# Kernel tuning notes

Measured on AMD Instinct MI355X. Metric: run time of the kernel, lower is better.

## Reference

```python
import jax, jax.numpy as jnp
import numpy as np

DIM = 512
HEADS = 8
HEAD_DIM = 64
INNER = HEADS * HEAD_DIM  # 512
FF = DIM * 2
EPS = 1e-5


def layernorm(x, g, b):
    mu = jnp.mean(x, axis=-1, keepdims=True)
    var = jnp.var(x, axis=-1, keepdims=True)
    return (x - mu) * jax.lax.rsqrt(var + EPS) * g + b


def setup_inputs() -> dict:
    key = jax.random.key(0)
    ks = jax.random.split(key, 10)
    s = lambda fan_in: 1.0 / np.sqrt(fan_in)
    return {
        "x": jax.random.normal(ks[0], (4, 2048, DIM), dtype=jnp.float32),
        "ln1_g": jnp.ones((DIM,), jnp.float32),
        "ln1_b": jnp.zeros((DIM,), jnp.float32),
        "w_qkv": jax.random.normal(ks[1], (DIM, 3 * INNER), jnp.float32) * s(DIM),
        "w_out": jax.random.normal(ks[2], (INNER, DIM), jnp.float32) * s(INNER),
        "b_out": jnp.zeros((DIM,), jnp.float32),
        "ln2_g": jnp.ones((DIM,), jnp.float32),
        "ln2_b": jnp.zeros((DIM,), jnp.float32),
        "w1": jax.random.normal(ks[3], (DIM, FF), jnp.float32) * s(DIM),
        "b1": jnp.zeros((FF,), jnp.float32),
        "w2": jax.random.normal(ks[4], (FF, DIM), jnp.float32) * s(FF),
        "b2": jnp.zeros((DIM,), jnp.float32),
    }


def reference(x, ln1_g, ln1_b, w_qkv, w_out, b_out, ln2_g, ln2_b, w1, b1, w2, b2):
    b, n, _ = x.shape
    # --- pre-LN MHSA ---
    h = layernorm(x, ln1_g, ln1_b)
    qkv = h @ w_qkv  # [b, n, 3*inner]
    q, k, v = jnp.split(qkv, 3, axis=-1)
    to_heads = lambda t: t.reshape(b, n, HEADS, HEAD_DIM).transpose(0, 2, 1, 3)
    q, k, v = to_heads(q), to_heads(k), to_heads(v)
    scores = jnp.einsum('bhid,bhjd->bhij', q, k) * (HEAD_DIM ** -0.5)
    attn = jax.nn.softmax(scores, axis=-1)
    attended = jnp.einsum('bhij,bhjd->bhid', attn, v)
    attended = attended.transpose(0, 2, 1, 3).reshape(b, n, INNER)
    x = attended @ w_out + b_out + x
    # --- pre-LN MLP ---
    h = layernorm(x, ln2_g, ln2_b)
    h = jax.nn.gelu(h @ w1 + b1, approximate=False)
    x = h @ w2 + b2 + x
    return x
```

## Files before the change

### kernel.cpp

```cpp
#include <hip/hip_runtime.h>
#include <math.h>


#define TOKENS 8192
#define SEQ    2048
typedef unsigned short u16;
typedef __attribute__((ext_vector_type(8))) _Float16 h8;
typedef __attribute__((ext_vector_type(4))) float f32x4;
typedef __attribute__((ext_vector_type(4))) unsigned short u16x4;

__device__ __forceinline__ u16 f2h(float f) {
    _Float16 h = (_Float16)f;
    return __builtin_bit_cast(u16, h);
}
__device__ __forceinline__ unsigned int pk2h(float a, float b) {
    return __builtin_bit_cast(unsigned int, __builtin_amdgcn_cvt_pkrtz(a, b));
}
__device__ __forceinline__ void a16(void* lds, const void* g) {
    __builtin_amdgcn_global_load_lds(
        (const __attribute__((address_space(1))) unsigned int*)g,
        (__attribute__((address_space(3))) unsigned int*)lds, 16, 0, 0);
}
__device__ __forceinline__ float gelu_exact(float v) {
    return 0.5f * v * (1.0f + erff(v * 0.70710678118654752f));
}

__global__ __launch_bounds__(256) void prep_k(const float* __restrict__ wqkv,
                                              const float* __restrict__ wout,
                                              const float* __restrict__ w1,
                                              const float* __restrict__ w2,
                                              u16* __restrict__ dqkv,
                                              u16* __restrict__ dout,
                                              u16* __restrict__ d1,
                                              u16* __restrict__ d2,
                                              const float* __restrict__ x,
                                              const float* __restrict__ g,
                                              const float* __restrict__ bta,
                                              u16* __restrict__ oh) {
    const int tid = threadIdx.x;
    if (blockIdx.x >= 512) {
        const int lane = tid & 63;
        const int row  = ((blockIdx.x - 512) << 2) + (tid >> 6);
        const float* xr = x + ((size_t)row << 9) + (lane << 3);
        float v[8];
        *(float4*)&v[0] = *(const float4*)xr;
        *(float4*)&v[4] = *(const float4*)(xr + 4);
        float s = 0.f, ss = 0.f;
#pragma unroll
        for (int i = 0; i < 8; i++) { s += v[i]; ss += v[i] * v[i]; }
#pragma unroll
        for (int m = 32; m; m >>= 1) {
            s  += __shfl_xor(s, m, 64);
            ss += __shfl_xor(ss, m, 64);
        }
        const float mu   = s * (1.0f / 512.0f);
        const float rstd = rsqrtf(ss * (1.0f / 512.0f) - mu * mu + 1e-5f);
        float gg[8], bb[8];
        *(float4*)&gg[0] = *(const float4*)(g + (lane << 3));
        *(float4*)&gg[4] = *(const float4*)(g + (lane << 3) + 4);
        *(float4*)&bb[0] = *(const float4*)(bta + (lane << 3));
        *(float4*)&bb[4] = *(const float4*)(bta + (lane << 3) + 4);
        union { u16 us[8]; uint4 q; } H;
#pragma unroll
        for (int i = 0; i < 8; i++) H.us[i] = f2h((v[i] - mu) * rstd * gg[i] + bb[i]);
        *(uint4*)&oh[((size_t)row << 9) + (lane << 3)] = H.q;
        return;
    }
    __shared__ float t[64][65];
    int b = blockIdx.x;
    const float* src; u16* dst; int K, N, n0, k0;
    if (b < 192)      { src = wqkv; dst = dqkv; K = 512;  N = 1536; n0 = (b % 24) << 6; k0 = (b / 24) << 6; }
    else if (b < 256) { b -= 192; src = wout; dst = dout; K = 512;  N = 512;  n0 = (b & 7) << 6;  k0 = (b >> 3) << 6; }
    else if (b < 384) { b -= 256; src = w1;   dst = d1;   K = 512;  N = 1024; n0 = (b & 15) << 6; k0 = (b >> 4) << 6; }
    else              { b -= 384; src = w2;   dst = d2;   K = 1024; N = 512;  n0 = (b & 7) << 6;  k0 = (b >> 3) << 6; }
    {
        const int kr = tid >> 2, nc = (tid & 3) << 4;
        const float* p = src + (size_t)(k0 + kr) * N + n0 + nc;
#pragma unroll
        for (int i = 0; i < 4; i++)
            *(float4*)&t[kr][nc + (i << 2)] = *(const float4*)(p + (i << 2));
    }
    __syncthreads();
    {
        const int nr = tid >> 2, kc = (tid & 3) << 4;
        union { u16 us[16]; uint4 q[2]; } H;
#pragma unroll
        for (int i = 0; i < 16; i++) H.us[i] = f2h(t[kc + i][nr]);
        const size_t o = (size_t)(n0 + nr) * K + k0 + kc;
        *(uint4*)&dst[o] = H.q[0];
        *(uint4*)&dst[o + 8] = H.q[1];
    }
}

__global__ __launch_bounds__(256) void ln_k(const float* __restrict__ x,
                                            const float* __restrict__ g,
                                            const float* __restrict__ bta,
                                            u16* __restrict__ oh) {
    const int lane = threadIdx.x & 63;
    const int row  = (blockIdx.x << 2) + (threadIdx.x >> 6);
    const float* xr = x + ((size_t)row << 9) + (lane << 3);
    float v[8];
    *(float4*)&v[0] = *(const float4*)xr;
    *(float4*)&v[4] = *(const float4*)(xr + 4);
    float s = 0.f, ss = 0.f;
#pragma unroll
    for (int i = 0; i < 8; i++) { s += v[i]; ss += v[i] * v[i]; }
#pragma unroll
    for (int m = 32; m; m >>= 1) {
        s  += __shfl_xor(s, m, 64);
        ss += __shfl_xor(ss, m, 64);
    }
    const float mu   = s * (1.0f / 512.0f);
    const float rstd = rsqrtf(ss * (1.0f / 512.0f) - mu * mu + 1e-5f);
    float gg[8], bb[8];
    *(float4*)&gg[0] = *(const float4*)(g + (lane << 3));
    *(float4*)&gg[4] = *(const float4*)(g + (lane << 3) + 4);
    *(float4*)&bb[0] = *(const float4*)(bta + (lane << 3));
    *(float4*)&bb[4] = *(const float4*)(bta + (lane << 3) + 4);
    union { u16 us[8]; uint4 q; } H;
#pragma unroll
    for (int i = 0; i < 8; i++) H.us[i] = f2h((v[i] - mu) * rstd * gg[i] + bb[i]);
    *(uint4*)&oh[((size_t)row << 9) + (lane << 3)] = H.q;
}

template <int EPI>
__global__ __launch_bounds__(256, 3) void sgemm_k(
    const u16* __restrict__ A, const u16* __restrict__ B,
    const float* __restrict__ bias, const float* __restrict__ res,
    float* __restrict__ Cf, u16* __restrict__ Ch, u16* __restrict__ Dh,
    int M, int N, int K) {
    __shared__ u16 sm[24576];
    const int tid = threadIdx.x;
    const int lane = tid & 63, wv = tid >> 6;
    const int col = lane & 15, quad = lane >> 4;
    const int wm = (wv & 1) << 6, wn = (wv >> 1) << 6;
    const int bm = blockIdx.y << 7, bn = blockIdx.x << 7;

    const int r0 = tid >> 2,         c0 = (tid & 3) ^ ((r0 >> 1) & 3);
    const int r1 = (tid + 256) >> 2, c1 = (tid & 3) ^ ((r1 >> 1) & 3);
    const u16* Ag0 = A + (size_t)(bm + r0) * K + c0 * 8;
    const u16* Ag1 = A + (size_t)(bm + r1) * K + c1 * 8;
    const u16* Bg0 = B + (size_t)(bn + r0) * K + c0 * 8;
    const u16* Bg1 = B + (size_t)(bn + r1) * K + c1 * 8;
    const int lw0 = wv * 512, lw1 = wv * 512 + 2048;
    const int swz = (col >> 1) & 3;
    const f32x4 z4 = {0.f, 0.f, 0.f, 0.f};
    f32x4 acc[4][4] = {{z4,z4,z4,z4},{z4,z4,z4,z4},{z4,z4,z4,z4},{z4,z4,z4,z4}};

    a16(&sm[lw0],        Ag0);       a16(&sm[lw1],        Ag1);
    a16(&sm[lw0 + 4096], Bg0);       a16(&sm[lw1 + 4096], Bg1);
    a16(&sm[8192 + lw0],        Ag0 + 32);  a16(&sm[8192 + lw1],        Ag1 + 32);
    a16(&sm[8192 + lw0 + 4096], Bg0 + 32);  a16(&sm[8192 + lw1 + 4096], Bg1 + 32);

    int cb = 0;
    int nb = 16384;
    for (int k0 = 0; k0 < K; k0 += 32) {
        if (k0 + 32 < K) {
            asm volatile("s_waitcnt vmcnt(4) lgkmcnt(0)\n\ts_barrier" ::: "memory");
        } else {
            asm volatile("s_waitcnt vmcnt(0) lgkmcnt(0)\n\ts_barrier" ::: "memory");
        }
        if (k0 + 64 < K) {
            const int kn = k0 + 64;
            a16(&sm[nb + lw0],        Ag0 + kn);  a16(&sm[nb + lw1],        Ag1 + kn);
            a16(&sm[nb + lw0 + 4096], Bg0 + kn);  a16(&sm[nb + lw1 + 4096], Bg1 + kn);
        }
        h8 af[4];
#pragma unroll
        for (int mt = 0; mt < 4; mt++) {
            const int ra = cb + (wm + (mt << 4) + col) * 32 + ((quad ^ swz) << 3);
            af[mt] = *(const h8*)&sm[ra];
        }
#pragma unroll
        for (int nt = 0; nt < 4; nt++) {
            const int rb = cb + 4096 + (wn + (nt << 4) + col) * 32 + ((quad ^ swz) << 3);
            h8 bf = *(const h8*)&sm[rb];
#pragma unroll
            for (int mt = 0; mt < 4; mt++)
                acc[mt][nt] = __builtin_amdgcn_mfma_f32_16x16x32_f16(af[mt], bf, acc[mt][nt], 0, 0, 0);
        }
        nb = cb;
        cb = (cb == 16384) ? 0 : cb + 8192;
    }

    if constexpr (EPI == 0) {
        if (bn >= 1024) {
            const int hd0  = (bn - 1024) >> 6;
            const int b8   = (bm >> 11) << 3;
            const int keyb = bm & 2047;
            __syncthreads();
#pragma unroll
            for (int hf = 0; hf < 2; hf++) {
                if ((wv >> 1) == hf) {
#pragma unroll
                    for (int mt = 0; mt < 4; mt++)
#pragma unroll
                    for (int rr = 0; rr < 4; rr++) {
                        const int key = wm + (mt << 4) + (quad << 2) + rr;
#pragma unroll
                        for (int nt = 0; nt < 4; nt++) {
                            const int dl = (nt << 4) + col;
                            sm[dl * 136 + key] = f2h(acc[mt][nt][rr]);
                        }
                    }
                }
                __syncthreads();
                {
                    const int d = tid >> 2;
#pragma unroll
                    for (int c = 0; c < 4; c++) {
                        const int key0 = ((((tid & 3) << 2) + c) << 3);
                        const size_t gb = ((size_t)(b8 + hd0 + hf) << 17)
                                        + ((size_t)d << 11) + keyb + key0;
                        *(uint4*)&Dh[gb] = *(const uint4*)&sm[d * 136 + key0];
                    }
                }
                __syncthreads();
            }
            return;
        }
    }

    float bs[4];
    if constexpr (EPI >= 1) {
#pragma unroll
        for (int nt = 0; nt < 4; nt++) bs[nt] = bias[bn + wn + (nt << 4) + col];
    }
#pragma unroll
    for (int mt = 0; mt < 4; mt++) {
#pragma unroll
        for (int rr = 0; rr < 4; rr++) {
            const int row = bm + wm + (mt << 4) + (quad << 2) + rr;
#pragma unroll
            for (int nt = 0; nt < 4; nt++) {
                const int colg = bn + wn + (nt << 4) + col;
                float v = acc[mt][nt][rr];
                if constexpr (EPI == 0) {
                    const int b = row >> 11, key = row & 2047;
                    if (bn < 512) {
                        Cf[((size_t)row << 9) + colg] = v;
                    } else {
                        const int hd = (colg - 512) >> 6, d = colg & 63;
                        Ch[((size_t)((b << 3) + hd) << 17) + (key << 6) + d] = f2h(v);
                    }
                } else if constexpr (EPI == 2) {
                    Ch[(size_t)row * N + colg] = f2h(gelu_exact(v + bs[nt]));
                } else {
                    const size_t o = (size_t)row * N + colg;
                    Cf[o] = v + bs[nt] + res[o];
                }
            }
        }
    }
}

__global__ __launch_bounds__(256, 4) void attn_k(const float* __restrict__ q,
                                                 const u16* __restrict__ kh,
                                                 const u16* __restrict__ vth,
                                                 u16* __restrict__ ah) {
    __shared__ u16 sm[20480];
    const int tid = threadIdx.x;
    const int lane = tid & 63, wv = tid >> 6;
    const int col = lane & 15, quad = lane >> 4;
    const int qt = blockIdx.x, bh = blockIdx.y;
    const int b = bh >> 3, h = bh & 7;
    const size_t tok0 = (size_t)b * SEQ;
    const size_t bhK = (size_t)bh << 17;
    const int q0 = qt << 6;

    h8 qf[2];
    {
        const int qrow = q0 + (wv << 4) + col;
        const float* qp = q + ((tok0 + qrow) << 9) + (h << 6) + (quad << 3);
#pragma unroll
        for (int kc = 0; kc < 2; kc++) {
            float v[8];
            *(float4*)&v[0] = *(const float4*)(qp + (kc << 5));
            *(float4*)&v[4] = *(const float4*)(qp + (kc << 5) + 4);
            union { u16 us[8]; h8 v8; } H;
#pragma unroll
            for (int i = 0; i < 8; i++) H.us[i] = f2h(v[i] * 0.125f);
            qf[kc] = H.v8;
        }
    }

    const f32x4 z4 = {0.f, 0.f, 0.f, 0.f};
    f32x4 o[4] = {z4, z4, z4, z4};
    float m_run = -1e30f, l_run = 0.f;

    size_t kbz[2], vbz[2];
    int doff[2];
#pragma unroll
    for (int j = 0; j < 2; j++) {
        const int C = (((j << 2) + wv) << 6) + lane;
        const int sr = C >> 3, sp = (C & 7) ^ (sr & 7);
        kbz[j] = bhK + ((size_t)sr << 6) + (sp << 3);
        vbz[j] = bhK + ((size_t)sr << 11) + (sp << 3);
        doff[j] = (((j << 2) + wv) << 9);
    }

#pragma unroll
    for (int j = 0; j < 2; j++) a16(&sm[doff[j]], kh + kbz[j]);
#pragma unroll
    for (int j = 0; j < 2; j++) a16(&sm[8192 + doff[j]], vth + vbz[j]);
#pragma unroll
    for (int j = 0; j < 2; j++) a16(&sm[4096 + doff[j]], kh + kbz[j] + 4096);

    int ib = 0;
    const int prow = (wv << 4) + col;
    const int p64 = prow << 6, p7 = prow & 7;
    for (int jt = 0; jt < 32; jt++, ib ^= 1) {
        if (jt < 31) {
            asm volatile("s_waitcnt vmcnt(2) lgkmcnt(0)\n\ts_barrier" ::: "memory");
        } else {
            asm volatile("s_waitcnt vmcnt(0) lgkmcnt(0)\n\ts_barrier" ::: "memory");
        }
        if (jt < 31) {
            const size_t vo = (size_t)(jt + 1) << 6;
            const int vb = 8192 + ((ib ^ 1) << 12);
#pragma unroll
            for (int j = 0; j < 2; j++) a16(&sm[vb + doff[j]], vth + vbz[j] + vo);
        }

        const int cb = ib << 12;
        f32x4 st[4] = {z4, z4, z4, z4};
        __builtin_amdgcn_s_setprio(1);
#pragma unroll
        for (int kb = 0; kb < 4; kb++) {
            const int key = (kb << 4) + col;
            const int r64 = key << 6, k7 = key & 7;
#pragma unroll
            for (int kc = 0; kc < 2; kc++) {
                const int ofs = cb + r64 + ((((kc << 2) + quad) ^ k7) << 3);
                h8 kf = *(const h8*)&sm[ofs];
                st[kb] = __builtin_amdgcn_mfma_f32_16x16x32_f16(kf, qf[kc], st[kb], 0, 0, 0);
            }
        }
        __builtin_amdgcn_s_setprio(0);

        float mx = st[0][0];
#pragma unroll
        for (int kb = 0; kb < 4; kb++)
#pragma unroll
            for (int r = 0; r < 4; r++) mx = fmaxf(mx, st[kb][r]);
        mx = fmaxf(mx, __shfl_xor(mx, 16));
        mx = fmaxf(mx, __shfl_xor(mx, 32));
        if (__any(mx > m_run + 7.5f)) {
            const float mn  = fmaxf(m_run, mx);
            const float alp = __expf(m_run - mn);
            m_run = mn;
            l_run *= alp;
            float aO[4];
#pragma unroll
            for (int r = 0; r < 4; r++) aO[r] = __shfl(alp, (quad << 2) + r);
#pragma unroll
            for (int db = 0; db < 4; db++) {
                o[db][0] *= aO[0]; o[db][1] *= aO[1];
                o[db][2] *= aO[2]; o[db][3] *= aO[3];
            }
        }
        float p[16];
        float rs = 0.0f;
#pragma unroll
        for (int kb = 0; kb < 4; kb++)
#pragma unroll
            for (int r = 0; r < 4; r++) {
                float e = __expf(st[kb][r] - m_run);
                p[(kb << 2) + r] = e;
                rs += e;
            }
        rs += __shfl_xor(rs, 16);
        rs += __shfl_xor(rs, 32);
        l_run += rs;
#pragma unroll
        for (int kb = 0; kb < 4; kb++) {
            uint2 w;
            w.x = pk2h(p[(kb << 2) + 0], p[(kb << 2) + 1]);
            w.y = pk2h(p[(kb << 2) + 2], p[(kb << 2) + 3]);
            const int c = (kb << 1) + (quad >> 1);
            *(uint2*)&sm[16384 + p64 + ((c ^ p7) << 3) + ((quad & 1) << 2)] = w;
        }

        asm volatile("s_waitcnt lgkmcnt(0)\n\ts_barrier" ::: "memory");

        if (jt < 30) {
            const size_t ko = (size_t)(jt + 2) << 12;
            const int kb2 = ib << 12;
#pragma unroll
            for (int j = 0; j < 2; j++) a16(&sm[kb2 + doff[j]], kh + kbz[j] + ko);
        }

        h8 pf[2];
#pragma unroll
        for (int kc = 0; kc < 2; kc++)
            pf[kc] = *(const h8*)&sm[16384 + p64 + ((((kc << 2) + quad) ^ p7) << 3)];

        const int vbase = 8192 + (ib << 12);
        __builtin_amdgcn_s_setprio(1);
#pragma unroll
        for (int db = 0; db < 4; db++) {
            const int d = (db << 4) + col;
            const int v64 = vbase + (d << 6), d7 = d & 7;
#pragma unroll
            for (int kc = 0; kc < 2; kc++) {
                h8 vf = *(const h8*)&sm[v64 + ((((kc << 2) + quad) ^ d7) << 3)];
                o[db] = __builtin_amdgcn_mfma_f32_16x16x32_f16(pf[kc], vf, o[db], 0, 0, 0);
            }
        }
        __builtin_amdgcn_s_setprio(0);
    }

    float linv[4];
#pragma unroll
    for (int r = 0; r < 4; r++) linv[r] = 1.0f / __shfl(l_run, (quad << 2) + r);
#pragma unroll
    for (int r = 0; r < 4; r++) {
        const size_t rowo = ((tok0 + q0 + (wv << 4) + (quad << 2) + r) << 9)
                            + (h << 6) + col;
#pragma unroll
        for (int db = 0; db < 4; db++)
            ah[rowo + (db << 4)] = f2h(o[db][r] * linv[r]);
    }
}

extern "C" void kernel_launch(void* const* d_in, const int* in_sizes, int n_in,
                              void* d_out, int out_size, void* d_ws, size_t ws_size,
                              hipStream_t stream) {
    const float* x     = (const float*)d_in[0];
    const float* ln1_g = (const float*)d_in[1];
    const float* ln1_b = (const float*)d_in[2];
    const float* w_qkv = (const float*)d_in[3];
    const float* w_out = (const float*)d_in[4];
    const float* b_out = (const float*)d_in[5];
    const float* ln2_g = (const float*)d_in[6];
    const float* ln2_b = (const float*)d_in[7];
    const float* w1    = (const float*)d_in[8];
    const float* b1    = (const float*)d_in[9];
    const float* w2    = (const float*)d_in[10];
    const float* b2    = (const float*)d_in[11];
    float* out = (float*)d_out;

    u16* wqkvh = (u16*)d_ws;
    u16* wouth = wqkvh + 1536 * 512;
    u16* w1h   = wouth + 512 * 512;
    u16* w2h   = w1h + 1024 * 512;
    u16* hbuf  = w2h + 512 * 1024;
    float* qbuf = (float*)(hbuf + (size_t)TOKENS * 512);
    float* x2   = qbuf;
    u16* kh  = (u16*)(qbuf + (size_t)TOKENS * 512);
    u16* vth = kh + (size_t)32 * 131072;
    u16* gh  = kh;

    prep_k<<<2560, 256, 0, stream>>>(w_qkv, w_out, w1, w2, wqkvh, wouth, w1h, w2h,
                                     x, ln1_g, ln1_b, hbuf);
    sgemm_k<0><<<dim3(12, 64), 256, 0, stream>>>(hbuf, wqkvh, nullptr, nullptr,
                                                 qbuf, kh, vth, TOKENS, 1536, 512);
    attn_k<<<dim3(32, 32), 256, 0, stream>>>(qbuf, kh, vth, hbuf);
    sgemm_k<1><<<dim3(4, 64), 256, 0, stream>>>(hbuf, wouth, b_out, x,
                                                x2, nullptr, nullptr, TOKENS, 512, 512);
    ln_k<<<TOKENS / 4, 256, 0, stream>>>(x2, ln2_g, ln2_b, hbuf);
    sgemm_k<2><<<dim3(8, 64), 256, 0, stream>>>(hbuf, w1h, b1, nullptr,
                                                nullptr, gh, nullptr, TOKENS, 1024, 512);
    sgemm_k<3><<<dim3(4, 64), 256, 0, stream>>>(gh, w2h, b2, x2,
                                                out, nullptr, nullptr, TOKENS, 512, 1024);
}
```

Baseline: 238.2 us.

## Double attention query tile per block to reuse K/V loads across two subtiles

Each attention block now handles 128 query rows instead of 64, with every wave processing two 16-row subtiles that share each K and V fragment read from shared memory. This halves the K/V global-to-LDS traffic and the barrier count per query row. In exchange the grid halves to 512 blocks, register pressure rises (launch bounds reduced to 2 blocks per SM), and the LDS buffer grows to hold the larger P tile.

```diff
diff --git a/kernel.cpp b/kernel.cpp
--- a/kernel.cpp
+++ b/kernel.cpp
@@ -254,11 +254,11 @@
     }
 }
 
-__global__ __launch_bounds__(256, 4) void attn_k(const float* __restrict__ q,
+__global__ __launch_bounds__(256, 2) void attn_k(const float* __restrict__ q,
                                                  const u16* __restrict__ kh,
                                                  const u16* __restrict__ vth,
                                                  u16* __restrict__ ah) {
-    __shared__ u16 sm[20480];
+    __shared__ u16 sm[24576];
     const int tid = threadIdx.x;
     const int lane = tid & 63, wv = tid >> 6;
     const int col = lane & 15, quad = lane >> 4;
@@ -266,11 +266,12 @@
     const int b = bh >> 3, h = bh & 7;
     const size_t tok0 = (size_t)b * SEQ;
     const size_t bhK = (size_t)bh << 17;
-    const int q0 = qt << 6;
-
-    h8 qf[2];
-    {
-        const int qrow = q0 + (wv << 4) + col;
+    const int q0 = qt << 7;
+
+    h8 qf[2][2];
+#pragma unroll
+    for (int sub = 0; sub < 2; sub++) {
+        const int qrow = q0 + (wv << 5) + (sub << 4) + col;
         const float* qp = q + ((tok0 + qrow) << 9) + (h << 6) + (quad << 3);
 #pragma unroll
         for (int kc = 0; kc < 2; kc++) {
@@ -280,13 +281,13 @@
             union { u16 us[8]; h8 v8; } H;
 #pragma unroll
             for (int i = 0; i < 8; i++) H.us[i] = f2h(v[i] * 0.125f);
-            qf[kc] = H.v8;
+            qf[sub][kc] = H.v8;
         }
     }
 
     const f32x4 z4 = {0.f, 0.f, 0.f, 0.f};
-    f32x4 o[4] = {z4, z4, z4, z4};
-    float m_run = -1e30f, l_run = 0.f;
+    f32x4 o[2][4] = {{z4, z4, z4, z4}, {z4, z4, z4, z4}};
+    float m_run[2] = {-1e30f, -1e30f}, l_run[2] = {0.f, 0.f};
 
     size_t kbz[2], vbz[2];
     int doff[2];
@@ -307,8 +308,6 @@
     for (int j = 0; j < 2; j++) a16(&sm[4096 + doff[j]], kh + kbz[j] + 4096);
 
     int ib = 0;
-    const int prow = (wv << 4) + col;
-    const int p64 = prow << 6, p7 = prow & 7;
     for (int jt = 0; jt < 32; jt++, ib ^= 1) {
         if (jt < 31) {
             asm volatile("s_waitcnt vmcnt(2) lgkmcnt(0)\n\ts_barrier" ::: "memory");
@@ -323,7 +322,7 @@
         }
 
         const int cb = ib << 12;
-        f32x4 st[4] = {z4, z4, z4, z4};
+        f32x4 st0[4] = {z4, z4, z4, z4}, st1[4] = {z4, z4, z4, z4};
         __builtin_amdgcn_s_setprio(1);
 #pragma unroll
         for (int kb = 0; kb < 4; kb++) {
@@ -333,52 +332,59 @@
             for (int kc = 0; kc < 2; kc++) {
                 const int ofs = cb + r64 + ((((kc << 2) + quad) ^ k7) << 3);
                 h8 kf = *(const h8*)&sm[ofs];
-                st[kb] = __builtin_amdgcn_mfma_f32_16x16x32_f16(kf, qf[kc], st[kb], 0, 0, 0);
+                st0[kb] = __builtin_amdgcn_mfma_f32_16x16x32_f16(kf, qf[0][kc], st0[kb], 0, 0, 0);
+                st1[kb] = __builtin_amdgcn_mfma_f32_16x16x32_f16(kf, qf[1][kc], st1[kb], 0, 0, 0);
             }
         }
         __builtin_amdgcn_s_setprio(0);
 
-        float mx = st[0][0];
-#pragma unroll
-        for (int kb = 0; kb < 4; kb++)
-#pragma unroll
-            for (int r = 0; r < 4; r++) mx = fmaxf(mx, st[kb][r]);
-        mx = fmaxf(mx, __shfl_xor(mx, 16));
-        mx = fmaxf(mx, __shfl_xor(mx, 32));
-        if (__any(mx > m_run + 7.5f)) {
-            const float mn  = fmaxf(m_run, mx);
-            const float alp = __expf(m_run - mn);
-            m_run = mn;
-            l_run *= alp;
-            float aO[4];
-#pragma unroll
-            for (int r = 0; r < 4; r++) aO[r] = __shfl(alp, (quad << 2) + r);
-#pragma unroll
-            for (int db = 0; db < 4; db++) {
-                o[db][0] *= aO[0]; o[db][1] *= aO[1];
-                o[db][2] *= aO[2]; o[db][3] *= aO[3];
-            }
-        }
-        float p[16];
-        float rs = 0.0f;
-#pragma unroll
-        for (int kb = 0; kb < 4; kb++)
-#pragma unroll
-            for (int r = 0; r < 4; r++) {
-                float e = __expf(st[kb][r] - m_run);
-                p[(kb << 2) + r] = e;
-                rs += e;
-            }
-        rs += __shfl_xor(rs, 16);
-        rs += __shfl_xor(rs, 32);
-        l_run += rs;
-#pragma unroll
-        for (int kb = 0; kb < 4; kb++) {
-            uint2 w;
-            w.x = pk2h(p[(kb << 2) + 0], p[(kb << 2) + 1]);
-            w.y = pk2h(p[(kb << 2) + 2], p[(kb << 2) + 3]);
-            const int c = (kb << 1) + (quad >> 1);
-            *(uint2*)&sm[16384 + p64 + ((c ^ p7) << 3) + ((quad & 1) << 2)] = w;
+#pragma unroll
+        for (int sub = 0; sub < 2; sub++) {
+            f32x4* st = sub ? st1 : st0;
+            const int prow = (wv << 5) + (sub << 4) + col;
+            const int p64 = prow << 6, p7 = prow & 7;
+            float mx = st[0][0];
+#pragma unroll
+            for (int kb = 0; kb < 4; kb++)
+#pragma unroll
+                for (int r = 0; r < 4; r++) mx = fmaxf(mx, st[kb][r]);
+            mx = fmaxf(mx, __shfl_xor(mx, 16));
+            mx = fmaxf(mx, __shfl_xor(mx, 32));
+            if (__any(mx > m_run[sub] + 7.5f)) {
+                const float mn  = fmaxf(m_run[sub], mx);
+                const float alp = __expf(m_run[sub] - mn);
+                m_run[sub] = mn;
+                l_run[sub] *= alp;
+                float aO[4];
+#pragma unroll
+                for (int r = 0; r < 4; r++) aO[r] = __shfl(alp, (quad << 2) + r);
+#pragma unroll
+                for (int db = 0; db < 4; db++) {
+                    o[sub][db][0] *= aO[0]; o[sub][db][1] *= aO[1];
+                    o[sub][db][2] *= aO[2]; o[sub][db][3] *= aO[3];
+                }
+            }
+            float p[16];
+            float rs = 0.0f;
+#pragma unroll
+            for (int kb = 0; kb < 4; kb++)
+#pragma unroll
+                for (int r = 0; r < 4; r++) {
+                    float e = __expf(st[kb][r] - m_run[sub]);
+                    p[(kb << 2) + r] = e;
+                    rs += e;
+                }
+            rs += __shfl_xor(rs, 16);
+            rs += __shfl_xor(rs, 32);
+            l_run[sub] += rs;
+#pragma unroll
+            for (int kb = 0; kb < 4; kb++) {
+                uint2 w;
+                w.x = pk2h(p[(kb << 2) + 0], p[(kb << 2) + 1]);
+                w.y = pk2h(p[(kb << 2) + 2], p[(kb << 2) + 3]);
+                const int c = (kb << 1) + (quad >> 1);
+                *(uint2*)&sm[16384 + p64 + ((c ^ p7) << 3) + ((quad & 1) << 2)] = w;
+            }
         }
 
         asm volatile("s_waitcnt lgkmcnt(0)\n\ts_barrier" ::: "memory");
@@ -390,10 +396,15 @@
             for (int j = 0; j < 2; j++) a16(&sm[kb2 + doff[j]], kh + kbz[j] + ko);
         }
 
-        h8 pf[2];
-#pragma unroll
-        for (int kc = 0; kc < 2; kc++)
-            pf[kc] = *(const h8*)&sm[16384 + p64 + ((((kc << 2) + quad) ^ p7) << 3)];
+        h8 pf[2][2];
+#pragma unroll
+        for (int sub = 0; sub < 2; sub++) {
+            const int prow = (wv << 5) + (sub << 4) + col;
+            const int p64 = prow << 6, p7 = prow & 7;
+#pragma unroll
+            for (int kc = 0; kc < 2; kc++)
+                pf[sub][kc] = *(const h8*)&sm[16384 + p64 + ((((kc << 2) + quad) ^ p7) << 3)];
+        }
 
         const int vbase = 8192 + (ib << 12);
         __builtin_amdgcn_s_setprio(1);
@@ -404,22 +415,26 @@
 #pragma unroll
             for (int kc = 0; kc < 2; kc++) {
                 h8 vf = *(const h8*)&sm[v64 + ((((kc << 2) + quad) ^ d7) << 3)];
-                o[db] = __builtin_amdgcn_mfma_f32_16x16x32_f16(pf[kc], vf, o[db], 0, 0, 0);
+                o[0][db] = __builtin_amdgcn_mfma_f32_16x16x32_f16(pf[0][kc], vf, o[0][db], 0, 0, 0);
+                o[1][db] = __builtin_amdgcn_mfma_f32_16x16x32_f16(pf[1][kc], vf, o[1][db], 0, 0, 0);
             }
         }
         __builtin_amdgcn_s_setprio(0);
     }
 
-    float linv[4];
-#pragma unroll
-    for (int r = 0; r < 4; r++) linv[r] = 1.0f / __shfl(l_run, (quad << 2) + r);
-#pragma unroll
-    for (int r = 0; r < 4; r++) {
-        const size_t rowo = ((tok0 + q0 + (wv << 4) + (quad << 2) + r) << 9)
-                            + (h << 6) + col;
-#pragma unroll
-        for (int db = 0; db < 4; db++)
-            ah[rowo + (db << 4)] = f2h(o[db][r] * linv[r]);
+#pragma unroll
+    for (int sub = 0; sub < 2; sub++) {
+        float linv[4];
+#pragma unroll
+        for (int r = 0; r < 4; r++) linv[r] = 1.0f / __shfl(l_run[sub], (quad << 2) + r);
+#pragma unroll
+        for (int r = 0; r < 4; r++) {
+            const size_t rowo = ((tok0 + q0 + (wv << 5) + (sub << 4) + (quad << 2) + r) << 9)
+                                + (h << 6) + col;
+#pragma unroll
+            for (int db = 0; db < 4; db++)
+                ah[rowo + (db << 4)] = f2h(o[sub][db][r] * linv[r]);
+        }
     }
 }
 
@@ -455,7 +470,7 @@
                                      x, ln1_g, ln1_b, hbuf);
     sgemm_k<0><<<dim3(12, 64), 256, 0, stream>>>(hbuf, wqkvh, nullptr, nullptr,
                                                  qbuf, kh, vth, TOKENS, 1536, 512);
-    attn_k<<<dim3(32, 32), 256, 0, stream>>>(qbuf, kh, vth, hbuf);
+    attn_k<<<dim3(16, 32), 256, 0, stream>>>(qbuf, kh, vth, hbuf);
     sgemm_k<1><<<dim3(4, 64), 256, 0, stream>>>(hbuf, wouth, b_out, x,
                                                 x2, nullptr, nullptr, TOKENS, 512, 512);
     ln_k<<<TOKENS / 4, 256, 0, stream>>>(x2, ln2_g, ln2_b, hbuf);
```

After: 235.1 us. About the same (-1.3%).
